# Optimization experiments

Hardware: AMD Instinct MI355X
Metric: run time of the kernel (lower is better)

Reference implementation:

```python
import jax, jax.numpy as jnp
import numpy as np

EPS = 1e-07
ALPHA, BETA, GAMMA = 0.8, 0.2, 0.1
N_NODES = 1_000_000
N_EDGES = 4_000_000


def setup_inputs() -> dict:
    key = jax.random.key(0)
    ks = jax.random.split(key, 11)
    return {
        "pred_ef": jax.random.normal(ks[0], (N_NODES, 2), dtype=jnp.float32),
        "target_y": jax.random.normal(ks[1], (N_NODES, 4), dtype=jnp.float32),
        "mask": jax.random.uniform(ks[2], (N_NODES, 4), dtype=jnp.float32),
        "edge_index": jax.random.randint(ks[3], (2, N_EDGES), 0, N_NODES, dtype=jnp.int32),
        "edge_attr": jax.random.normal(ks[4], (N_EDGES, 2), dtype=jnp.float32),
        "bus_type": jax.random.randint(ks[5], (N_NODES,), 0, 3, dtype=jnp.int32),
        "target_vm": jax.random.uniform(ks[6], (N_NODES,), dtype=jnp.float32),
        "xymean": jax.random.normal(ks[7], (1, 4), dtype=jnp.float32),
        "xystd": jax.random.uniform(ks[8], (1, 4), dtype=jnp.float32),
        "edgemean": jax.random.normal(ks[9], (1, 2), dtype=jnp.float32),
        "edgestd": jax.random.uniform(ks[10], (1, 2), dtype=jnp.float32),
    }


def reference(pred_ef, target_y, mask, edge_index, edge_attr, bus_type, target_vm,
              xymean, xystd, edgemean, edgestd):
    n = pred_ef.shape[0]

    # ---- masked MSE on (e, f) ----
    target_ef = target_y[:, 2:]
    mask_ef = mask[:, 2:]
    loss_mse = jnp.sum((pred_ef - target_ef) ** 2 * mask_ef) / (jnp.sum(mask_ef) + 1e-06)

    # ---- physics loss (rectangular power imbalance) ----
    real_pq = target_y[:, :2] * (xystd[:, :2] + EPS) + xymean[:, :2]
    real_edge = edge_attr * (edgestd + EPS) + edgemean
    # duplicate edges reversed (directed input -> make undirected), as in the torch branch
    idx_i = jnp.concatenate([edge_index[0], edge_index[1]])  # aggregation target (flow=target_to_source)
    idx_j = jnp.concatenate([edge_index[1], edge_index[0]])
    ea = jnp.concatenate([real_edge, real_edge], axis=0)     # [2E, 2]

    x_i = pred_ef[idx_i]  # [2E, 2] gather
    x_j = pred_ef[idx_j]
    e_i, f_i = x_i[:, 0], x_i[:, 1]
    e_j, f_j = x_j[:, 0], x_j[:, 1]
    g_ij, b_ij = ea[:, 0], ea[:, 1]

    term1 = e_i * e_j + f_i * f_j
    term2 = f_i * e_j - e_i * f_j
    v_sq = e_i ** 2 + f_i ** 2
    P_flow = g_ij * (v_sq - term1) - b_ij * term2
    Q_flow = -b_ij * (v_sq - term1) - g_ij * term2
    msg = jnp.stack([P_flow, Q_flow], axis=-1)               # [2E, 2]

    calc_pq_flow = jax.ops.segment_sum(msg, idx_i, num_segments=n)  # scatter-add
    loss_phys = jnp.mean((real_pq + calc_pq_flow) ** 2)

    # ---- PV-bus voltage-magnitude loss ----
    ef_real = pred_ef * (xystd[:, 2:] + EPS) + xymean[:, 2:]
    vm_sq_pred = ef_real[:, 0] ** 2 + ef_real[:, 1] ** 2
    is_pv = (bus_type == 1).astype(pred_ef.dtype)
    cnt = jnp.sum(is_pv)
    pv_sum = jnp.sum(jnp.abs(vm_sq_pred - target_vm ** 2) * is_pv)
    loss_pv = jnp.where(cnt > 0, pv_sum / jnp.maximum(cnt, 1.0), 0.0)

    total = ALPHA * loss_mse + BETA * loss_phys + GAMMA * loss_pv
    return total, loss_mse, loss_phys, loss_pv
```

## Files before the change

### kernel.cpp

```cpp
#include <hip/hip_runtime.h>
#include <hip/hip_fp16.h>
#include <math.h>

#define EPSF 1e-7f

#define K3GRID  512
#define K3BLK   1024
#define K4BLK   1024
#define MAXBINS 512

#define PB_NEW  11
#define PSZ_NEW (1 << PB_NEW)
#define CAPF    44

struct Scalars { double mse_num, mse_den, pv_sum, pv_cnt, phys_sum; };

typedef float f2v __attribute__((ext_vector_type(2)));
typedef float f4v __attribute__((ext_vector_type(4)));
typedef int   i2v __attribute__((ext_vector_type(2)));
typedef unsigned u2v __attribute__((ext_vector_type(2)));

__device__ __forceinline__ float2 nt_ld_f2(const float2* p) {
    f2v v = __builtin_nontemporal_load((const f2v*)p);
    return make_float2(v.x, v.y);
}
__device__ __forceinline__ float4 nt_ld_f4(const float4* p) {
    f4v v = __builtin_nontemporal_load((const f4v*)p);
    return make_float4(v.x, v.y, v.z, v.w);
}
__device__ __forceinline__ int2 nt_ld_i2(const int2* p) {
    i2v v = __builtin_nontemporal_load((const i2v*)p);
    return make_int2(v.x, v.y);
}
__device__ __forceinline__ uint2 nt_ld_u2(const uint2* p) {
    u2v v = __builtin_nontemporal_load((const u2v*)p);
    return make_uint2(v.x, v.y);
}
__device__ __forceinline__ int nt_ld_i(const int* p) {
    return __builtin_nontemporal_load(p);
}
__device__ __forceinline__ float nt_ld_f(const float* p) {
    return __builtin_nontemporal_load(p);
}

__global__ void zero_scalars_kernel(double* s) {
    int i = threadIdx.x;
    if (i < 5) s[i] = 0.0;
}

__global__ void zero_f32_kernel(float* p, int n) {
    int stride = gridDim.x * blockDim.x;
    for (int i = blockIdx.x * blockDim.x + threadIdx.x; i < n; i += stride)
        p[i] = 0.0f;
}

__device__ double blockReduceSum(double v) {
    __shared__ double red[16];
    #pragma unroll
    for (int off = 32; off > 0; off >>= 1)
        v += __shfl_down(v, off, 64);
    int lane = threadIdx.x & 63;
    int wid  = threadIdx.x >> 6;
    __syncthreads();
    if (lane == 0) red[wid] = v;
    __syncthreads();
    if (threadIdx.x == 0) {
        double s = 0.0;
        int nw = blockDim.x >> 6;
        for (int w = 0; w < nw; ++w) s += red[w];
        v = s;
    }
    return v;
}

__device__ __forceinline__ void msg_compute(float2 ps, float2 po, float2 at,
                                            float es0, float es1, float em0, float em1,
                                            float& P, float& Q)
{
    float g  = at.x * es0 + em0;
    float bb = at.y * es1 + em1;
    float t1 = ps.x * po.x + ps.y * po.y;
    float t2 = ps.y * po.x - ps.x * po.y;
    float vs = ps.x * ps.x + ps.y * ps.y;
    P =  g  * (vs - t1) - bb * t2;
    Q = -bb * (vs - t1) - g  * t2;
}

__global__ void pass1_nodes(const float2* __restrict__ pred,
                            const float4* __restrict__ ty,
                            const float4* __restrict__ mask,
                            const int*    __restrict__ bus,
                            const float*  __restrict__ tvm,
                            const float*  __restrict__ xymean,
                            const float*  __restrict__ xystd,
                            float2*       __restrict__ calc,
                            Scalars* sc, int n, int seed_calc)
{
    float xs0 = xystd[0] + EPSF, xs1 = xystd[1] + EPSF;
    float xs2 = xystd[2] + EPSF, xs3 = xystd[3] + EPSF;
    float xm0 = xymean[0], xm1 = xymean[1], xm2 = xymean[2], xm3 = xymean[3];

    double mse_num = 0.0, mse_den = 0.0, pv_sum = 0.0, pv_cnt = 0.0;
    int stride = gridDim.x * blockDim.x;
    for (int i = blockIdx.x * blockDim.x + threadIdx.x; i < n; i += stride) {
        float2 p = pred[i];
        float4 t = nt_ld_f4(&ty[i]);
        float4 m = nt_ld_f4(&mask[i]);
        float d0 = p.x - t.z, d1 = p.y - t.w;
        mse_num += (double)(d0 * d0 * m.z + d1 * d1 * m.w);
        mse_den += (double)(m.z + m.w);
        calc[i] = seed_calc ? make_float2(t.x * xs0 + xm0, t.y * xs1 + xm1)
                            : make_float2(0.0f, 0.0f);
        float er0 = p.x * xs2 + xm2;
        float er1 = p.y * xs3 + xm3;
        float vmsq = er0 * er0 + er1 * er1;
        if (nt_ld_i(&bus[i]) == 1) {
            float tv = nt_ld_f(&tvm[i]);
            pv_sum += (double)fabsf(vmsq - tv * tv);
            pv_cnt += 1.0;
        }
    }
    mse_num = blockReduceSum(mse_num);
    mse_den = blockReduceSum(mse_den);
    pv_sum  = blockReduceSum(pv_sum);
    pv_cnt  = blockReduceSum(pv_cnt);
    if (threadIdx.x == 0) {
        atomicAdd(&sc->mse_num, mse_num);
        atomicAdd(&sc->mse_den, mse_den);
        atomicAdd(&sc->pv_sum,  pv_sum);
        atomicAdd(&sc->pv_cnt,  pv_cnt);
    }
}


__global__ __launch_bounds__(K3BLK)
void scatter_h2(const int*    __restrict__ ei,
                const float2* __restrict__ ea,
                const float2* __restrict__ pred,
                const float*  __restrict__ emean,
                const float*  __restrict__ estd,
                uint2*        __restrict__ bkt,
                unsigned int* __restrict__ gcnt,
                float*        __restrict__ calc,
                int nE, int nbins)
{
    __shared__ unsigned int lcnt[MAXBINS];
    for (int i = threadIdx.x; i < nbins; i += blockDim.x) lcnt[i] = 0;
    __syncthreads();

    float es0 = estd[0] + EPSF, es1 = estd[1] + EPSF;
    float em0 = emean[0], em1 = emean[1];

    int tid = blockIdx.x * blockDim.x + threadIdx.x;
    int stride = gridDim.x * blockDim.x;
    int npair = nE >> 1;

    #define EMIT(SELF, OTHER, G, B, HGB)                                         \
        do {                                                                     \
            int bin = (SELF) >> PB_NEW;                                          \
            unsigned r = atomicAdd(&lcnt[bin], 1u);                              \
            if (r < (unsigned)CAPF) {                                            \
                uint2 rec;                                                       \
                rec.x = ((unsigned)((SELF) & (PSZ_NEW - 1)) << 20) |             \
                        (unsigned)(OTHER);                                       \
                rec.y = (HGB);                                                   \
                bkt[((size_t)blockIdx.x * nbins + bin) * CAPF + r] = rec;        \
            } else {                                                             \
                float2 ps = pred[SELF];                                          \
                float2 po = pred[OTHER];                                         \
                float t1 = ps.x * po.x + ps.y * po.y;                            \
                float t2 = ps.y * po.x - ps.x * po.y;                            \
                float vs = ps.x * ps.x + ps.y * ps.y;                            \
                float P =  (G) * (vs - t1) - (B) * t2;                           \
                float Q = -(B) * (vs - t1) - (G) * t2;                           \
                unsafeAtomicAdd(&calc[2 * (size_t)(SELF)],     P);               \
                unsafeAtomicAdd(&calc[2 * (size_t)(SELF) + 1], Q);               \
            }                                                                    \
        } while (0)

    for (int q = tid; q < npair; q += stride) {
        int2 av = nt_ld_i2(&((const int2*)ei)[q]);
        int2 bv = nt_ld_i2(&((const int2*)(ei + nE))[q]);
        float4 e2 = nt_ld_f4(&((const float4*)ea)[q]);
        float g0 = e2.x * es0 + em0, b0 = e2.y * es1 + em1;
        float g1 = e2.z * es0 + em0, b1 = e2.w * es1 + em1;
        unsigned h0 = __builtin_bit_cast(unsigned, __floats2half2_rn(g0, b0));
        unsigned h1 = __builtin_bit_cast(unsigned, __floats2half2_rn(g1, b1));
        EMIT(av.x, bv.x, g0, b0, h0);
        EMIT(bv.x, av.x, g0, b0, h0);
        EMIT(av.y, bv.y, g1, b1, h1);
        EMIT(bv.y, av.y, g1, b1, h1);
    }
    if ((nE & 1) && tid == 0) {
        int k = nE - 1;
        int a = ei[k], b = ei[nE + k];
        float2 at = ea[k];
        float g = at.x * es0 + em0, bb = at.y * es1 + em1;
        unsigned h = __builtin_bit_cast(unsigned, __floats2half2_rn(g, bb));
        EMIT(a, b, g, bb, h);
        EMIT(b, a, g, bb, h);
    }
    #undef EMIT

    __syncthreads();
    for (int i = threadIdx.x; i < nbins; i += blockDim.x)
        gcnt[(size_t)blockIdx.x * nbins + i] = min(lcnt[i], (unsigned)CAPF);
}

__global__ __launch_bounds__(K4BLK)
void gather_fused(const uint2*        __restrict__ bkt,
                  const unsigned int* __restrict__ gcnt,
                  const float2* __restrict__ pred,
                  const float*  __restrict__ calc,
                  const float4* __restrict__ ty,
                  const float4* __restrict__ mask,
                  const int*    __restrict__ bus,
                  const float*  __restrict__ tvm,
                  const float*  __restrict__ xymean,
                  const float*  __restrict__ xystd,
                  Scalars* sc, int n, int nbins)
{
    __shared__ float accx[PSZ_NEW];
    __shared__ float accy[PSZ_NEW];
    __shared__ float2 plds[PSZ_NEW];
    __shared__ unsigned int cnts[K3GRID];

    int p = blockIdx.x;
    int base = p << PB_NEW;
    for (int i = threadIdx.x; i < PSZ_NEW; i += blockDim.x) {
        accx[i] = 0.0f; accy[i] = 0.0f;
        int g = base + i;
        plds[i] = (g < n) ? pred[g] : make_float2(0.0f, 0.0f);
    }
    for (int b = threadIdx.x; b < K3GRID; b += blockDim.x)
        cnts[b] = gcnt[(size_t)b * nbins + p];
    __syncthreads();

    const int slots = K3GRID * CAPF;
    for (int f = threadIdx.x; f < slots; f += blockDim.x) {
        int b = f / CAPF;
        int t = f - b * CAPF;
        if ((unsigned)t < cnts[b]) {
            uint2 rec = nt_ld_u2(&bkt[((size_t)b * nbins + p) * CAPF + t]);
            int o   = (int)(rec.x & 0xFFFFFu);
            int lid = (int)(rec.x >> 20);
            __half2 h2 = __builtin_bit_cast(__half2, rec.y);
            float g  = __low2float(h2);
            float bb = __high2float(h2);
            float2 po = pred[o];
            float2 ps = plds[lid];
            float t1 = ps.x * po.x + ps.y * po.y;
            float t2 = ps.y * po.x - ps.x * po.y;
            float vs = ps.x * ps.x + ps.y * ps.y;
            float P =  g  * (vs - t1) - bb * t2;
            float Q = -bb * (vs - t1) - g  * t2;
            atomicAdd(&accx[lid], P);
            atomicAdd(&accy[lid], Q);
        }
    }
    __syncthreads();

    float xs0 = xystd[0] + EPSF, xs1 = xystd[1] + EPSF;
    float xs2 = xystd[2] + EPSF, xs3 = xystd[3] + EPSF;
    float xm0 = xymean[0], xm1 = xymean[1], xm2 = xymean[2], xm3 = xymean[3];

    double mse_num = 0.0, mse_den = 0.0, pv_sum = 0.0, pv_cnt = 0.0, phys = 0.0;
    for (int i = threadIdx.x; i < PSZ_NEW; i += blockDim.x) {
        int g = base + i;
        if (g < n) {
            float2 pp = plds[i];
            float4 t = nt_ld_f4(&ty[g]);
            float4 m = nt_ld_f4(&mask[g]);
            float d0 = pp.x - t.z, d1 = pp.y - t.w;
            mse_num += (double)(d0 * d0 * m.z + d1 * d1 * m.w);
            mse_den += (double)(m.z + m.w);
            float er0 = pp.x * xs2 + xm2;
            float er1 = pp.y * xs3 + xm3;
            float vmsq = er0 * er0 + er1 * er1;
            if (nt_ld_i(&bus[g]) == 1) {
                float tv = nt_ld_f(&tvm[g]);
                pv_sum += (double)fabsf(vmsq - tv * tv);
                pv_cnt += 1.0;
            }
            float2 ov = ((const float2*)calc)[g];
            float vx = t.x * xs0 + xm0 + accx[i] + ov.x;
            float vy = t.y * xs1 + xm1 + accy[i] + ov.y;
            phys += (double)vx * (double)vx + (double)vy * (double)vy;
        }
    }
    mse_num = blockReduceSum(mse_num);
    mse_den = blockReduceSum(mse_den);
    pv_sum  = blockReduceSum(pv_sum);
    pv_cnt  = blockReduceSum(pv_cnt);
    phys    = blockReduceSum(phys);
    if (threadIdx.x == 0) {
        atomicAdd(&sc->mse_num, mse_num);
        atomicAdd(&sc->mse_den, mse_den);
        atomicAdd(&sc->pv_sum,  pv_sum);
        atomicAdd(&sc->pv_cnt,  pv_cnt);
        atomicAdd(&sc->phys_sum, phys);
    }
}


__global__ void pass2_edges(const int*    __restrict__ ei,
                            const float2* __restrict__ ea,
                            const float2* __restrict__ pred,
                            const float*  __restrict__ emean,
                            const float*  __restrict__ estd,
                            float*        __restrict__ calc,
                            int nE)
{
    float es0 = estd[0] + EPSF, es1 = estd[1] + EPSF;
    float em0 = emean[0], em1 = emean[1];
    int stride = gridDim.x * blockDim.x;
    for (int k = blockIdx.x * blockDim.x + threadIdx.x; k < nE; k += stride) {
        int a = ei[k];
        int b = ei[nE + k];
        float2 at = ea[k];
        float2 pa = pred[a];
        float2 pb = pred[b];
        float Pa, Qa, Pb, Qb;
        msg_compute(pa, pb, at, es0, es1, em0, em1, Pa, Qa);
        msg_compute(pb, pa, at, es0, es1, em0, em1, Pb, Qb);
        unsafeAtomicAdd(&calc[2 * (size_t)a],     Pa);
        unsafeAtomicAdd(&calc[2 * (size_t)a + 1], Qa);
        unsafeAtomicAdd(&calc[2 * (size_t)b],     Pb);
        unsafeAtomicAdd(&calc[2 * (size_t)b + 1], Qb);
    }
}

__global__ void pass3_phys(const float2* __restrict__ calc, Scalars* sc, int n)
{
    double s = 0.0;
    int stride = gridDim.x * blockDim.x;
    for (int i = blockIdx.x * blockDim.x + threadIdx.x; i < n; i += stride) {
        float2 c = calc[i];
        s += (double)c.x * (double)c.x + (double)c.y * (double)c.y;
    }
    s = blockReduceSum(s);
    if (threadIdx.x == 0) atomicAdd(&sc->phys_sum, s);
}

__global__ void finalize_kernel(const Scalars* __restrict__ sc, float* __restrict__ out, int n)
{
    if (threadIdx.x == 0 && blockIdx.x == 0) {
        double mse  = sc->mse_num / (sc->mse_den + 1e-6);
        double phys = sc->phys_sum / (2.0 * (double)n);
        double pv   = (sc->pv_cnt > 0.0) ? (sc->pv_sum / fmax(sc->pv_cnt, 1.0)) : 0.0;
        double total = 0.8 * mse + 0.2 * phys + 0.1 * pv;
        out[0] = (float)total;
        out[1] = (float)mse;
        out[2] = (float)phys;
        out[3] = (float)pv;
    }
}

extern "C" void kernel_launch(void* const* d_in, const int* in_sizes, int n_in,
                              void* d_out, int out_size, void* d_ws, size_t ws_size,
                              hipStream_t stream) {
    const float2* pred   = (const float2*)d_in[0];
    const float4* ty     = (const float4*)d_in[1];
    const float4* mask   = (const float4*)d_in[2];
    const int*    ei     = (const int*)d_in[3];
    const float2* ea     = (const float2*)d_in[4];
    const int*    bus    = (const int*)d_in[5];
    const float*  tvm    = (const float*)d_in[6];
    const float*  xymean = (const float*)d_in[7];
    const float*  xystd  = (const float*)d_in[8];
    const float*  emean  = (const float*)d_in[9];
    const float*  estd   = (const float*)d_in[10];
    float* out = (float*)d_out;

    int n  = in_sizes[0] / 2;
    int nE = in_sizes[3] / 2;

    char* basep = (char*)d_ws;
    Scalars* sc = (Scalars*)basep;
    size_t head = 64;
    float* calc = (float*)(basep + head);
    head += (size_t)2 * n * sizeof(float);
    head = (head + 15) & ~(size_t)15;

    const int BLK = 256, GRID = 2048;

    int nbinsN = (n + PSZ_NEW - 1) >> PB_NEW;
    size_t slotsN = (size_t)K3GRID * nbinsN;
    size_t offN = head + slotsN * sizeof(unsigned int);
    offN = (offN + 15) & ~(size_t)15;
    size_t needN = offN + slotsN * (size_t)CAPF * sizeof(uint2);
    bool useNew = (n <= (1 << 20)) && (nbinsN <= MAXBINS) && (needN <= ws_size);

    zero_scalars_kernel<<<1, 64, 0, stream>>>((double*)sc);

    if (useNew) {
        unsigned int* gcnt = (unsigned int*)(basep + head);
        uint2* bkt = (uint2*)(basep + offN);

        zero_f32_kernel<<<1024, 256, 0, stream>>>(calc, 2 * n);
        scatter_h2<<<K3GRID, K3BLK, 0, stream>>>(ei, ea, pred, emean, estd,
                                                 bkt, gcnt, calc, nE, nbinsN);
        gather_fused<<<nbinsN, K4BLK, 0, stream>>>(bkt, gcnt, pred, calc, ty, mask,
                                                   bus, tvm, xymean, xystd, sc, n, nbinsN);
        finalize_kernel<<<1, 64, 0, stream>>>(sc, out, n);
        return;
    }

    pass1_nodes<<<GRID, BLK, 0, stream>>>(pred, ty, mask, bus, tvm, xymean, xystd,
                                          (float2*)calc, sc, n, 1);
    pass2_edges<<<GRID, BLK, 0, stream>>>(ei, ea, pred, emean, estd, calc, nE);
    pass3_phys<<<GRID, BLK, 0, stream>>>((const float2*)calc, sc, n);
    finalize_kernel<<<1, 64, 0, stream>>>(sc, out, n);
}
```

Measured before the change: 226.0 us.

## Compute edge messages in the scatter pass and bucket half-precision P/Q

Moves the power-flow message computation from the binned gather kernel into the scatter kernel. Both endpoint predictions are now loaded once per edge and reused for both directions. The bucket records now carry the local node id and the P/Q message packed as half2, instead of the other node id and packed g/b. The gather kernel then only does shared-memory atomic accumulation, and it drops its LDS staging of pred. The random pred loads now happen in the scatter phase, and rounding the messages themselves to fp16 may add precision error to the physics loss.

```diff
diff --git a/kernel.cpp b/kernel.cpp
--- a/kernel.cpp
+++ b/kernel.cpp
@@ -134,7 +134,7 @@
 
 
 __global__ __launch_bounds__(K3BLK)
-void scatter_h2(const int*    __restrict__ ei,
+void scatter_pq(const int*    __restrict__ ei,
                 const float2* __restrict__ ea,
                 const float2* __restrict__ pred,
                 const float*  __restrict__ emean,
@@ -155,26 +155,18 @@
     int stride = gridDim.x * blockDim.x;
     int npair = nE >> 1;
 
-    #define EMIT(SELF, OTHER, G, B, HGB)                                         \
+    #define EMITPQ(SELF, P, Q)                                                   \
         do {                                                                     \
             int bin = (SELF) >> PB_NEW;                                          \
             unsigned r = atomicAdd(&lcnt[bin], 1u);                              \
             if (r < (unsigned)CAPF) {                                            \
                 uint2 rec;                                                       \
-                rec.x = ((unsigned)((SELF) & (PSZ_NEW - 1)) << 20) |             \
-                        (unsigned)(OTHER);                                       \
-                rec.y = (HGB);                                                   \
+                rec.x = (unsigned)((SELF) & (PSZ_NEW - 1));                      \
+                rec.y = __builtin_bit_cast(unsigned, __floats2half2_rn((P),(Q)));\
                 bkt[((size_t)blockIdx.x * nbins + bin) * CAPF + r] = rec;        \
             } else {                                                             \
-                float2 ps = pred[SELF];                                          \
-                float2 po = pred[OTHER];                                         \
-                float t1 = ps.x * po.x + ps.y * po.y;                            \
-                float t2 = ps.y * po.x - ps.x * po.y;                            \
-                float vs = ps.x * ps.x + ps.y * ps.y;                            \
-                float P =  (G) * (vs - t1) - (B) * t2;                           \
-                float Q = -(B) * (vs - t1) - (G) * t2;                           \
-                unsafeAtomicAdd(&calc[2 * (size_t)(SELF)],     P);               \
-                unsafeAtomicAdd(&calc[2 * (size_t)(SELF) + 1], Q);               \
+                unsafeAtomicAdd(&calc[2 * (size_t)(SELF)],     (P));             \
+                unsafeAtomicAdd(&calc[2 * (size_t)(SELF) + 1], (Q));             \
             }                                                                    \
         } while (0)
 
@@ -182,25 +174,35 @@
         int2 av = nt_ld_i2(&((const int2*)ei)[q]);
         int2 bv = nt_ld_i2(&((const int2*)(ei + nE))[q]);
         float4 e2 = nt_ld_f4(&((const float4*)ea)[q]);
-        float g0 = e2.x * es0 + em0, b0 = e2.y * es1 + em1;
-        float g1 = e2.z * es0 + em0, b1 = e2.w * es1 + em1;
-        unsigned h0 = __builtin_bit_cast(unsigned, __floats2half2_rn(g0, b0));
-        unsigned h1 = __builtin_bit_cast(unsigned, __floats2half2_rn(g1, b1));
-        EMIT(av.x, bv.x, g0, b0, h0);
-        EMIT(bv.x, av.x, g0, b0, h0);
-        EMIT(av.y, bv.y, g1, b1, h1);
-        EMIT(bv.y, av.y, g1, b1, h1);
+        float2 pa0 = pred[av.x];
+        float2 pb0 = pred[bv.x];
+        float2 pa1 = pred[av.y];
+        float2 pb1 = pred[bv.y];
+        float2 at0 = make_float2(e2.x, e2.y);
+        float2 at1 = make_float2(e2.z, e2.w);
+        float P, Q;
+        msg_compute(pa0, pb0, at0, es0, es1, em0, em1, P, Q);
+        EMITPQ(av.x, P, Q);
+        msg_compute(pb0, pa0, at0, es0, es1, em0, em1, P, Q);
+        EMITPQ(bv.x, P, Q);
+        msg_compute(pa1, pb1, at1, es0, es1, em0, em1, P, Q);
+        EMITPQ(av.y, P, Q);
+        msg_compute(pb1, pa1, at1, es0, es1, em0, em1, P, Q);
+        EMITPQ(bv.y, P, Q);
     }
     if ((nE & 1) && tid == 0) {
         int k = nE - 1;
         int a = ei[k], b = ei[nE + k];
         float2 at = ea[k];
-        float g = at.x * es0 + em0, bb = at.y * es1 + em1;
-        unsigned h = __builtin_bit_cast(unsigned, __floats2half2_rn(g, bb));
-        EMIT(a, b, g, bb, h);
-        EMIT(b, a, g, bb, h);
-    }
-    #undef EMIT
+        float2 pa = pred[a];
+        float2 pb = pred[b];
+        float P, Q;
+        msg_compute(pa, pb, at, es0, es1, em0, em1, P, Q);
+        EMITPQ(a, P, Q);
+        msg_compute(pb, pa, at, es0, es1, em0, em1, P, Q);
+        EMITPQ(b, P, Q);
+    }
+    #undef EMITPQ
 
     __syncthreads();
     for (int i = threadIdx.x; i < nbins; i += blockDim.x)
@@ -208,29 +210,26 @@
 }
 
 __global__ __launch_bounds__(K4BLK)
-void gather_fused(const uint2*        __restrict__ bkt,
-                  const unsigned int* __restrict__ gcnt,
-                  const float2* __restrict__ pred,
-                  const float*  __restrict__ calc,
-                  const float4* __restrict__ ty,
-                  const float4* __restrict__ mask,
-                  const int*    __restrict__ bus,
-                  const float*  __restrict__ tvm,
-                  const float*  __restrict__ xymean,
-                  const float*  __restrict__ xystd,
-                  Scalars* sc, int n, int nbins)
+void gather_pq(const uint2*        __restrict__ bkt,
+               const unsigned int* __restrict__ gcnt,
+               const float2* __restrict__ pred,
+               const float*  __restrict__ calc,
+               const float4* __restrict__ ty,
+               const float4* __restrict__ mask,
+               const int*    __restrict__ bus,
+               const float*  __restrict__ tvm,
+               const float*  __restrict__ xymean,
+               const float*  __restrict__ xystd,
+               Scalars* sc, int n, int nbins)
 {
     __shared__ float accx[PSZ_NEW];
     __shared__ float accy[PSZ_NEW];
-    __shared__ float2 plds[PSZ_NEW];
     __shared__ unsigned int cnts[K3GRID];
 
     int p = blockIdx.x;
     int base = p << PB_NEW;
     for (int i = threadIdx.x; i < PSZ_NEW; i += blockDim.x) {
         accx[i] = 0.0f; accy[i] = 0.0f;
-        int g = base + i;
-        plds[i] = (g < n) ? pred[g] : make_float2(0.0f, 0.0f);
     }
     for (int b = threadIdx.x; b < K3GRID; b += blockDim.x)
         cnts[b] = gcnt[(size_t)b * nbins + p];
@@ -242,20 +241,10 @@
         int t = f - b * CAPF;
         if ((unsigned)t < cnts[b]) {
             uint2 rec = nt_ld_u2(&bkt[((size_t)b * nbins + p) * CAPF + t]);
-            int o   = (int)(rec.x & 0xFFFFFu);
-            int lid = (int)(rec.x >> 20);
-            __half2 h2 = __builtin_bit_cast(__half2, rec.y);
-            float g  = __low2float(h2);
-            float bb = __high2float(h2);
-            float2 po = pred[o];
-            float2 ps = plds[lid];
-            float t1 = ps.x * po.x + ps.y * po.y;
-            float t2 = ps.y * po.x - ps.x * po.y;
-            float vs = ps.x * ps.x + ps.y * ps.y;
-            float P =  g  * (vs - t1) - bb * t2;
-            float Q = -bb * (vs - t1) - g  * t2;
-            atomicAdd(&accx[lid], P);
-            atomicAdd(&accy[lid], Q);
+            int lid = (int)rec.x;
+            __half2 pq = __builtin_bit_cast(__half2, rec.y);
+            atomicAdd(&accx[lid], __low2float(pq));
+            atomicAdd(&accy[lid], __high2float(pq));
         }
     }
     __syncthreads();
@@ -268,7 +257,7 @@
     for (int i = threadIdx.x; i < PSZ_NEW; i += blockDim.x) {
         int g = base + i;
         if (g < n) {
-            float2 pp = plds[i];
+            float2 pp = pred[g];
             float4 t = nt_ld_f4(&ty[g]);
             float4 m = nt_ld_f4(&mask[g]);
             float d0 = pp.x - t.z, d1 = pp.y - t.w;
@@ -398,10 +387,10 @@
         uint2* bkt = (uint2*)(basep + offN);
 
         zero_f32_kernel<<<1024, 256, 0, stream>>>(calc, 2 * n);
-        scatter_h2<<<K3GRID, K3BLK, 0, stream>>>(ei, ea, pred, emean, estd,
+        scatter_pq<<<K3GRID, K3BLK, 0, stream>>>(ei, ea, pred, emean, estd,
                                                  bkt, gcnt, calc, nE, nbinsN);
-        gather_fused<<<nbinsN, K4BLK, 0, stream>>>(bkt, gcnt, pred, calc, ty, mask,
-                                                   bus, tvm, xymean, xystd, sc, n, nbinsN);
+        gather_pq<<<nbinsN, K4BLK, 0, stream>>>(bkt, gcnt, pred, calc, ty, mask,
+                                                bus, tvm, xymean, xystd, sc, n, nbinsN);
         finalize_kernel<<<1, 64, 0, stream>>>(sc, out, n);
         return;
     }
```

After: 299.5 us. 1.33x slower.
